# Kernel tuning notes

Measured on AMD Instinct MI355X. Metric: run time of the kernel, lower is better.

Reference implementation:

```python
import jax, jax.numpy as jnp
import numpy as np
from jax import lax

EPS = 1e-06
K = 7  # kernel_size
C1 = 0.01 ** 2
C2 = 0.03 ** 2

_SOBEL_X = jnp.array([[-1.0, 0.0, 1.0], [-2.0, 0.0, 2.0], [-1.0, 0.0, 1.0]], dtype=jnp.float32).reshape(1, 1, 3, 3)
_SOBEL_Y = jnp.array([[-1.0, -2.0, -1.0], [0.0, 0.0, 0.0], [1.0, 2.0, 1.0]], dtype=jnp.float32).reshape(1, 1, 3, 3)


def _conv3x3(x, w):
    # NCHW cross-correlation with zero padding=1 (matches F.conv2d)
    return lax.conv_general_dilated(
        x, w, window_strides=(1, 1), padding=[(1, 1), (1, 1)],
        dimension_numbers=('NCHW', 'OIHW', 'NCHW'))


def _box(x):
    # avg_pool2d(k, stride=1, pad=k//2, count_include_pad=True):
    # sum over zero-padded window, divide by k*k everywhere.
    p = K // 2
    s = lax.reduce_window(x, jnp.float32(0.0), lax.add,
                          window_dimensions=(1, 1, K, K),
                          window_strides=(1, 1, 1, 1),
                          padding=[(0, 0), (0, 0), (p, p), (p, p)])
    return s / jnp.float32(K * K)


def _grad_mag(x):
    gx = _conv3x3(x, _SOBEL_X)
    gy = _conv3x3(x, _SOBEL_Y)
    return jnp.sqrt(gx * gx + gy * gy + EPS)


def setup_inputs() -> dict:
    key = jax.random.key(0)
    k1, k2 = jax.random.split(key)
    B, H, W = 64, 512, 512
    pred = jax.random.normal(k1, (B, 1, H, W), dtype=jnp.float32)
    target = jax.random.normal(k2, (B, 1, H, W), dtype=jnp.float32)
    min_target = jnp.zeros((B,), dtype=jnp.float32)
    max_target = jnp.ones((B,), dtype=jnp.float32)
    return {"pred": pred, "target": target, "min_target": min_target, "max_target": max_target}


def reference(pred, target, min_target, max_target):
    B = pred.shape[0]
    mn = min_target.reshape(B, 1, 1, 1)
    mx = max_target.reshape(B, 1, 1, 1)
    dr = jnp.maximum(mx - mn, EPS)
    p = (pred - mn) / dr
    t = (target - mn) / dr

    gp = _grad_mag(p)
    gt = _grad_mag(t)

    mu_p = _box(p)
    mu_t = _box(t)
    luminance = (2.0 * mu_p * mu_t + C1) / (mu_p * mu_p + mu_t * mu_t + C1)

    mu_gp = _box(gp)
    mu_gt = _box(gt)
    sig_p = _box(gp * gp) - mu_gp * mu_gp
    sig_t = _box(gt * gt) - mu_gt * mu_gt
    sig_x = _box(gp * gt) - mu_gp * mu_gt
    cs = (2.0 * sig_x + C2) / (sig_p + sig_t + C2)

    return 1.0 - jnp.mean(luminance * cs)
```

## Files before the change

### kernel.cpp

```cpp
#include <hip/hip_runtime.h>
#include <hip/hip_fp16.h>
#include <math.h>


constexpr int NT = 256;
constexpr float EPS_F = 1e-6f;
constexpr float C1S = 2401.0f * 0.0001f;
constexpr float C2S = 2401.0f * 0.0009f;

union U4 { uint4 u; __half2 h[4]; };
union F4U { float4 v; float a[4]; };

__device__ __forceinline__ __half2 h2swap(__half2 x) {
    unsigned u = __builtin_bit_cast(unsigned, x);
    u = (u >> 16) | (u << 16);
    return __builtin_bit_cast(__half2, u);
}

__device__ __forceinline__ float ssim_px(__half2 apt, __half2 ag, __half2 agg, __half2 agx) {
    float2 vpt = __half22float2(apt);
    float2 vg  = __half22float2(ag);
    float2 vgg = __half22float2(agg);
    float  vgx = __low2float(agx);
    float lum_n = 2.0f * vpt.x * vpt.y + C1S;
    float lum_d = vpt.x * vpt.x + vpt.y * vpt.y + C1S;
    float cs_n  = 2.0f * (49.0f * vgx - vg.x * vg.y) + C2S;
    float cs_d  = 49.0f * (vgg.x + vgg.y) - vg.x * vg.x - vg.y * vg.y + C2S;
    return lum_n * cs_n * __builtin_amdgcn_rcpf(lum_d) * __builtin_amdgcn_rcpf(cs_d);
}

__global__ __launch_bounds__(NT, 4)
void gssim_strip(const float* __restrict__ pred, const float* __restrict__ target,
                 const float* __restrict__ mn_arr, const float* __restrict__ mx_arr,
                 float* __restrict__ partial) {
    constexpr int H = 512, W = 512;
    __shared__ alignas(16) __half2 spt[40][44];
    __shared__ alignas(16) __half2 sg[38][44];
    __shared__ alignas(16) __half2 hsAll[32][41][4];
    __shared__ float red[4];

    const int blk = blockIdx.x;
    const int b   = blk >> 4;
    const int gy0 = (blk & 15) * 32;
    const int tid = threadIdx.x;

    const float mn     = mn_arr[b];
    const float inv_dr = 1.0f / fmaxf(mx_arr[b] - mn, EPS_F);
    const float* pimg = pred   + (size_t)b * H * W;
    const float* timg = target + (size_t)b * H * W;

    const int gS  = tid % 10;
    const int yr  = tid / 10;
    const int yS0 = 2 * yr, yS1 = yS0 + 1;
    const int gyS0 = gy0 - 4 + yS0;
    const int gyS1 = gyS0 + 1;
    const bool rok0 = (gyS0 >= 0 && gyS0 < H);
    const bool rok1 = (gyS1 >= 0 && gyS1 < H);
    const bool hasS = (tid < 200);

    F4U Pa0, Ta0, Pa1, Ta1;

    auto stage1 = [&](int gx0n, bool rowok, int gyI, F4U& P, F4U& T) {
        int gx = gx0n - 4 + 4 * gS;
        P.v = make_float4(0.f, 0.f, 0.f, 0.f);
        T.v = make_float4(0.f, 0.f, 0.f, 0.f);
        if (rowok) {
            if (gx >= 0 && gx + 4 <= W) {
                P.v = *reinterpret_cast<const float4*>(pimg + (size_t)gyI * W + gx);
                T.v = *reinterpret_cast<const float4*>(timg + (size_t)gyI * W + gx);
            } else {
#pragma unroll
                for (int c = 0; c < 4; ++c) {
                    int x = gx + c;
                    if (x >= 0 && x < W) {
                        P.a[c] = pimg[(size_t)gyI * W + x];
                        T.a[c] = timg[(size_t)gyI * W + x];
                    }
                }
            }
        }
    };
    auto stagePair = [&](int gx0n) {
        stage1(gx0n, rok0, gyS0, Pa0, Ta0);
        stage1(gx0n, rok1, gyS1, Pa1, Ta1);
    };

    auto writeOne = [&](F4U& P, F4U& T, int y, bool rowok, int gx0n) {
        int gx = gx0n - 4 + 4 * gS;
        U4 w;
#pragma unroll
        for (int c = 0; c < 4; ++c) {
            int x = gx + c;
            bool ok = rowok && (x >= 0) && (x < W);
            float pv = ok ? (P.a[c] - mn) * inv_dr : 0.f;
            float tv = ok ? (T.a[c] - mn) * inv_dr : 0.f;
            w.h[c] = __floats2half2_rn(pv, tv);
        }
        *reinterpret_cast<uint4*>(&spt[y][4 * gS]) = w.u;
    };
    auto writePair = [&](int gx0n) {
        writeOne(Pa0, Ta0, yS0, rok0, gx0n);
        writeOne(Pa1, Ta1, yS1, rok1, gx0n);
    };

    const __half2 two2  = __float2half2_rn(2.0f);
    const __half2 eps2  = __float2half2_rn(1e-6f);
    const __half2 zero2 = __float2half2_rn(0.0f);

    if (hasS) { stagePair(0); writePair(0); }
    __syncthreads();

    float accl = 0.0f;

    for (int tx = 0; tx < 16; ++tx) {
        const int gx0 = tx * 32;

        if (tx < 15 && hasS) stagePair(gx0 + 32);

        if (tid < 190) {
            const int g  = tid % 10, kr = tid / 10;
            const int j0 = 4 * g, k0 = 2 * kr;
            __half2 a[4][6];
#pragma unroll
            for (int r = 0; r < 4; ++r) {
                U4 v; v.u = *reinterpret_cast<const uint4*>(&spt[k0 + r][j0]);
                a[r][0] = v.h[0]; a[r][1] = v.h[1]; a[r][2] = v.h[2]; a[r][3] = v.h[3];
                uint2 v2 = *reinterpret_cast<const uint2*>(&spt[k0 + r][j0 + 4]);
                a[r][4] = __builtin_bit_cast(__half2, v2.x);
                a[r][5] = __builtin_bit_cast(__half2, v2.y);
            }
            bool cm[4];
#pragma unroll
            for (int c = 0; c < 4; ++c) {
                int gc = gx0 + j0 + c - 3;
                cm[c] = (gc >= 0 && gc < W);
            }
#pragma unroll
            for (int rr = 0; rr < 2; ++rr) {
                const int k = k0 + rr;
                const int gr = gy0 + k - 3;
                U4 w; w.h[0] = zero2; w.h[1] = zero2; w.h[2] = zero2; w.h[3] = zero2;
                if (gr >= 0 && gr < H) {
#pragma unroll
                    for (int c = 0; c < 4; ++c) {
                        __half2 gxh = __hsub2(a[rr][c + 2], a[rr][c]);
                        gxh = __hfma2(two2, __hsub2(a[rr + 1][c + 2], a[rr + 1][c]), gxh);
                        gxh = __hadd2(gxh, __hsub2(a[rr + 2][c + 2], a[rr + 2][c]));
                        __half2 gyh = __hsub2(a[rr + 2][c], a[rr][c]);
                        gyh = __hfma2(two2, __hsub2(a[rr + 2][c + 1], a[rr][c + 1]), gyh);
                        gyh = __hadd2(gyh, __hsub2(a[rr + 2][c + 2], a[rr][c + 2]));
                        __half2 m2 = __hfma2(gxh, gxh, __hfma2(gyh, gyh, eps2));
                        __half2 mag = h2sqrt(m2);
                        w.h[c] = cm[c] ? mag : zero2;
                    }
                }
                *reinterpret_cast<uint4*>(&sg[k][j0]) = w.u;
            }
        }
        __syncthreads();

        if (tid < 152) {
            const int kr = tid % 19, cg = tid / 19;
            const int c0 = 4 * cg;
#pragma unroll
            for (int rr = 0; rr < 2; ++rr) {
                const int k = 2 * kr + rr;
                __half2 ptv[12], sgv[12];
#pragma unroll
                for (int q = 0; q < 3; ++q) {
                    U4 v; v.u = *reinterpret_cast<const uint4*>(&spt[k + 1][c0 + 4 * q]);
                    ptv[4 * q] = v.h[0]; ptv[4 * q + 1] = v.h[1]; ptv[4 * q + 2] = v.h[2]; ptv[4 * q + 3] = v.h[3];
                    U4 u; u.u = *reinterpret_cast<const uint4*>(&sg[k][c0 + 4 * q]);
                    sgv[4 * q] = u.h[0]; sgv[4 * q + 1] = u.h[1]; sgv[4 * q + 2] = u.h[2]; sgv[4 * q + 3] = u.h[3];
                }
                __half2 gg[10], gx2[10];
#pragma unroll
                for (int q = 0; q < 10; ++q) {
                    gg[q]  = __hmul2(sgv[q], sgv[q]);
                    gx2[q] = __hmul2(sgv[q], h2swap(sgv[q]));
                }
                __half2 Hpt = ptv[1], Hg = sgv[0], Hgg = gg[0], Hgx = gx2[0];
#pragma unroll
                for (int q = 1; q < 7; ++q) {
                    Hpt = __hadd2(Hpt, ptv[q + 1]);
                    Hg  = __hadd2(Hg,  sgv[q]);
                    Hgg = __hadd2(Hgg, gg[q]);
                    Hgx = __hadd2(Hgx, gx2[q]);
                }
                U4 w0;
                w0.h[0] = Hpt; w0.h[1] = Hg; w0.h[2] = Hgg; w0.h[3] = Hgx;
                *reinterpret_cast<uint4*>(&hsAll[c0][k][0]) = w0.u;
#pragma unroll
                for (int m = 1; m < 4; ++m) {
                    Hpt = __hadd2(__hsub2(Hpt, ptv[m]),      ptv[m + 7]);
                    Hg  = __hadd2(__hsub2(Hg,  sgv[m - 1]),  sgv[m + 6]);
                    Hgg = __hadd2(__hsub2(Hgg, gg[m - 1]),   gg[m + 6]);
                    Hgx = __hadd2(__hsub2(Hgx, gx2[m - 1]),  gx2[m + 6]);
                    U4 w;
                    w.h[0] = Hpt; w.h[1] = Hg; w.h[2] = Hgg; w.h[3] = Hgx;
                    *reinterpret_cast<uint4*>(&hsAll[c0 + m][k][0]) = w.u;
                }
            }
        }
        __syncthreads();

        {
            const int ox = tid & 31;
            const int q  = tid >> 5;
            const int r0 = 4 * q;
            U4 win[10];
#pragma unroll
            for (int j = 0; j < 7; ++j)
                win[j].u = *reinterpret_cast<const uint4*>(&hsAll[ox][r0 + j][0]);
            __half2 Spt = win[0].h[0], Sg = win[0].h[1], Sgg = win[0].h[2], Sgx = win[0].h[3];
#pragma unroll
            for (int j = 1; j < 7; ++j) {
                Spt = __hadd2(Spt, win[j].h[0]);
                Sg  = __hadd2(Sg,  win[j].h[1]);
                Sgg = __hadd2(Sgg, win[j].h[2]);
                Sgx = __hadd2(Sgx, win[j].h[3]);
            }
            accl += ssim_px(Spt, Sg, Sgg, Sgx);
#pragma unroll
            for (int s = 1; s < 4; ++s) {
                win[6 + s].u = *reinterpret_cast<const uint4*>(&hsAll[ox][r0 + 6 + s][0]);
                Spt = __hadd2(__hsub2(Spt, win[s - 1].h[0]), win[6 + s].h[0]);
                Sg  = __hadd2(__hsub2(Sg,  win[s - 1].h[1]), win[6 + s].h[1]);
                Sgg = __hadd2(__hsub2(Sgg, win[s - 1].h[2]), win[6 + s].h[2]);
                Sgx = __hadd2(__hsub2(Sgx, win[s - 1].h[3]), win[6 + s].h[3]);
                accl += ssim_px(Spt, Sg, Sgg, Sgx);
            }
        }

        if (tx < 15 && hasS) writePair(gx0 + 32);
        __syncthreads();
    }

#pragma unroll
    for (int off = 32; off > 0; off >>= 1) accl += __shfl_down(accl, off, 64);
    if ((tid & 63) == 0) red[tid >> 6] = accl;
    __syncthreads();
    if (tid == 0) partial[blk] = red[0] + red[1] + red[2] + red[3];
}

__global__ __launch_bounds__(256)
void gssim_final(const float* __restrict__ partial, int n,
                 float* __restrict__ out, double inv_count) {
    __shared__ double sred[256];
    double acc = 0.0;
    for (int i = threadIdx.x; i < n; i += 256) acc += (double)partial[i];
    sred[threadIdx.x] = acc;
    __syncthreads();
    for (int s = 128; s > 0; s >>= 1) {
        if ((int)threadIdx.x < s) sred[threadIdx.x] += sred[threadIdx.x + s];
        __syncthreads();
    }
    if (threadIdx.x == 0) out[0] = (float)(1.0 - sred[0] * inv_count);
}

extern "C" void kernel_launch(void* const* d_in, const int* in_sizes, int n_in,
                              void* d_out, int out_size, void* d_ws, size_t ws_size,
                              hipStream_t stream) {
    const float* pred   = (const float*)d_in[0];
    const float* target = (const float*)d_in[1];
    const float* mn     = (const float*)d_in[2];
    const float* mx     = (const float*)d_in[3];
    float* out = (float*)d_out;

    const int B = in_sizes[2];
    const int H = 512, W = 512;

    float* partial = (float*)d_ws;

    const int nblocks = B * (H / 32);
    gssim_strip<<<nblocks, NT, 0, stream>>>(pred, target, mn, mx, partial);

    const double inv_count = 1.0 / ((double)B * (double)H * (double)W);
    gssim_final<<<1, 256, 0, stream>>>(partial, nblocks, out, inv_count);
}
```

Measured before the change: 79.81 us.

## Accumulate gradient second moments in fp32 via fdot2 with swizzled shared layout

Squared and cross gradient products are now formed with the packed fp16 dot-product instruction and accumulated in fp32 instead of fp16 half2 pairs. The horizontal-sum buffer is re-laid out row-major with an XOR-like rotation on the column index to change the bank access pattern. The SSIM epilogue merges two reciprocals into one. This cuts per-pixel packed operations and fp16 overflow or precision risk, at the cost of a slightly different layout and more fp32 adds.

After: 93.01 us. 16.5% more time.

```diff
diff --git a/kernel.cpp b/kernel.cpp
--- a/kernel.cpp
+++ b/kernel.cpp
@@ -10,6 +10,19 @@
 
 union U4 { uint4 u; __half2 h[4]; };
 union F4U { float4 v; float a[4]; };
+union HS { uint4 u; struct { __half2 pt; __half2 g; float gg; float gx; } s; };
+
+typedef _Float16 hvec2 __attribute__((ext_vector_type(2)));
+
+__device__ __forceinline__ float fdot2(__half2 a, __half2 b, float c) {
+#if __has_builtin(__builtin_amdgcn_fdot2)
+    return __builtin_amdgcn_fdot2(__builtin_bit_cast(hvec2, a),
+                                  __builtin_bit_cast(hvec2, b), c, false);
+#else
+    float2 fa = __half22float2(a), fb = __half22float2(b);
+    return c + fa.x * fb.x + fa.y * fb.y;
+#endif
+}
 
 __device__ __forceinline__ __half2 h2swap(__half2 x) {
     unsigned u = __builtin_bit_cast(unsigned, x);
@@ -17,16 +30,14 @@
     return __builtin_bit_cast(__half2, u);
 }
 
-__device__ __forceinline__ float ssim_px(__half2 apt, __half2 ag, __half2 agg, __half2 agx) {
+__device__ __forceinline__ float ssim_px(__half2 apt, __half2 ag, float sgg, float sgx) {
     float2 vpt = __half22float2(apt);
     float2 vg  = __half22float2(ag);
-    float2 vgg = __half22float2(agg);
-    float  vgx = __low2float(agx);
     float lum_n = 2.0f * vpt.x * vpt.y + C1S;
     float lum_d = vpt.x * vpt.x + vpt.y * vpt.y + C1S;
-    float cs_n  = 2.0f * (49.0f * vgx - vg.x * vg.y) + C2S;
-    float cs_d  = 49.0f * (vgg.x + vgg.y) - vg.x * vg.x - vg.y * vg.y + C2S;
-    return lum_n * cs_n * __builtin_amdgcn_rcpf(lum_d) * __builtin_amdgcn_rcpf(cs_d);
+    float cs_n  = 49.0f * sgx - 2.0f * vg.x * vg.y + C2S;
+    float cs_d  = 49.0f * sgg - vg.x * vg.x - vg.y * vg.y + C2S;
+    return lum_n * cs_n * __builtin_amdgcn_rcpf(lum_d * cs_d);
 }
 
 __global__ __launch_bounds__(NT, 4)
@@ -36,7 +47,7 @@
     constexpr int H = 512, W = 512;
     __shared__ alignas(16) __half2 spt[40][44];
     __shared__ alignas(16) __half2 sg[38][44];
-    __shared__ alignas(16) __half2 hsAll[32][41][4];
+    __shared__ alignas(16) HS hsAll[38][32];
     __shared__ float red[4];
 
     const int blk = blockIdx.x;
@@ -173,32 +184,33 @@
                     U4 u; u.u = *reinterpret_cast<const uint4*>(&sg[k][c0 + 4 * q]);
                     sgv[4 * q] = u.h[0]; sgv[4 * q + 1] = u.h[1]; sgv[4 * q + 2] = u.h[2]; sgv[4 * q + 3] = u.h[3];
                 }
-                __half2 gg[10], gx2[10];
+                float dgg[10], dgx[10];
 #pragma unroll
                 for (int q = 0; q < 10; ++q) {
-                    gg[q]  = __hmul2(sgv[q], sgv[q]);
-                    gx2[q] = __hmul2(sgv[q], h2swap(sgv[q]));
-                }
-                __half2 Hpt = ptv[1], Hg = sgv[0], Hgg = gg[0], Hgx = gx2[0];
+                    dgg[q] = fdot2(sgv[q], sgv[q], 0.0f);
+                    dgx[q] = fdot2(sgv[q], h2swap(sgv[q]), 0.0f);
+                }
+                __half2 Hpt = ptv[1], Hg = sgv[0];
+                float Hgg = dgg[0], Hgx = dgx[0];
 #pragma unroll
                 for (int q = 1; q < 7; ++q) {
                     Hpt = __hadd2(Hpt, ptv[q + 1]);
                     Hg  = __hadd2(Hg,  sgv[q]);
-                    Hgg = __hadd2(Hgg, gg[q]);
-                    Hgx = __hadd2(Hgx, gx2[q]);
-                }
-                U4 w0;
-                w0.h[0] = Hpt; w0.h[1] = Hg; w0.h[2] = Hgg; w0.h[3] = Hgx;
-                *reinterpret_cast<uint4*>(&hsAll[c0][k][0]) = w0.u;
+                    Hgg += dgg[q];
+                    Hgx += dgx[q];
+                }
+                HS w0;
+                w0.s.pt = Hpt; w0.s.g = Hg; w0.s.gg = Hgg; w0.s.gx = Hgx;
+                *reinterpret_cast<uint4*>(&hsAll[k][(c0 + k) & 31]) = w0.u;
 #pragma unroll
                 for (int m = 1; m < 4; ++m) {
-                    Hpt = __hadd2(__hsub2(Hpt, ptv[m]),      ptv[m + 7]);
-                    Hg  = __hadd2(__hsub2(Hg,  sgv[m - 1]),  sgv[m + 6]);
-                    Hgg = __hadd2(__hsub2(Hgg, gg[m - 1]),   gg[m + 6]);
-                    Hgx = __hadd2(__hsub2(Hgx, gx2[m - 1]),  gx2[m + 6]);
-                    U4 w;
-                    w.h[0] = Hpt; w.h[1] = Hg; w.h[2] = Hgg; w.h[3] = Hgx;
-                    *reinterpret_cast<uint4*>(&hsAll[c0 + m][k][0]) = w.u;
+                    Hpt = __hadd2(__hsub2(Hpt, ptv[m]),     ptv[m + 7]);
+                    Hg  = __hadd2(__hsub2(Hg,  sgv[m - 1]), sgv[m + 6]);
+                    Hgg += dgg[m + 6] - dgg[m - 1];
+                    Hgx += dgx[m + 6] - dgx[m - 1];
+                    HS w;
+                    w.s.pt = Hpt; w.s.g = Hg; w.s.gg = Hgg; w.s.gx = Hgx;
+                    *reinterpret_cast<uint4*>(&hsAll[k][(c0 + m + k) & 31]) = w.u;
                 }
             }
         }
@@ -208,26 +220,30 @@
             const int ox = tid & 31;
             const int q  = tid >> 5;
             const int r0 = 4 * q;
-            U4 win[10];
-#pragma unroll
-            for (int j = 0; j < 7; ++j)
-                win[j].u = *reinterpret_cast<const uint4*>(&hsAll[ox][r0 + j][0]);
-            __half2 Spt = win[0].h[0], Sg = win[0].h[1], Sgg = win[0].h[2], Sgx = win[0].h[3];
+            HS win[10];
+#pragma unroll
+            for (int j = 0; j < 7; ++j) {
+                int r = r0 + j;
+                win[j].u = *reinterpret_cast<const uint4*>(&hsAll[r][(ox + r) & 31]);
+            }
+            __half2 Spt = win[0].s.pt, Sg = win[0].s.g;
+            float Sgg = win[0].s.gg, Sgx = win[0].s.gx;
 #pragma unroll
             for (int j = 1; j < 7; ++j) {
-                Spt = __hadd2(Spt, win[j].h[0]);
-                Sg  = __hadd2(Sg,  win[j].h[1]);
-                Sgg = __hadd2(Sgg, win[j].h[2]);
-                Sgx = __hadd2(Sgx, win[j].h[3]);
+                Spt = __hadd2(Spt, win[j].s.pt);
+                Sg  = __hadd2(Sg,  win[j].s.g);
+                Sgg += win[j].s.gg;
+                Sgx += win[j].s.gx;
             }
             accl += ssim_px(Spt, Sg, Sgg, Sgx);
 #pragma unroll
             for (int s = 1; s < 4; ++s) {
-                win[6 + s].u = *reinterpret_cast<const uint4*>(&hsAll[ox][r0 + 6 + s][0]);
-                Spt = __hadd2(__hsub2(Spt, win[s - 1].h[0]), win[6 + s].h[0]);
-                Sg  = __hadd2(__hsub2(Sg,  win[s - 1].h[1]), win[6 + s].h[1]);
-                Sgg = __hadd2(__hsub2(Sgg, win[s - 1].h[2]), win[6 + s].h[2]);
-                Sgx = __hadd2(__hsub2(Sgx, win[s - 1].h[3]), win[6 + s].h[3]);
+                int r = r0 + 6 + s;
+                win[6 + s].u = *reinterpret_cast<const uint4*>(&hsAll[r][(ox + r) & 31]);
+                Spt = __hadd2(__hsub2(Spt, win[s - 1].s.pt), win[6 + s].s.pt);
+                Sg  = __hadd2(__hsub2(Sg,  win[s - 1].s.g),  win[6 + s].s.g);
+                Sgg += win[6 + s].s.gg - win[s - 1].s.gg;
+                Sgx += win[6 + s].s.gx - win[s - 1].s.gx;
                 accl += ssim_px(Spt, Sg, Sgg, Sgx);
             }
         }
```
